# Optimization experiments

Hardware: AMD Instinct MI355X
Metric: run time of the kernel (lower is better)

Reference implementation:

```python
import jax, jax.numpy as jnp
import numpy as np

B = 4096   # batch_size from init_kwargs
D = 128    # embedding dim
TEMP = 0.25


def _l2_normalize(x, eps=1e-12):
    # matches F.normalize(dim=1): x / max(||x||, eps)
    n = jnp.linalg.norm(x, axis=1, keepdims=True)
    return x / jnp.maximum(n, eps)


def setup_inputs() -> dict:
    key = jax.random.key(0)
    k1, k2 = jax.random.split(key)
    return {
        "emb_i": jax.random.normal(k1, (B, D), dtype=jnp.float32),
        "emb_j": jax.random.normal(k2, (B, D), dtype=jnp.float32),
    }


def reference(emb_i, emb_j):
    b = emb_i.shape[0]
    z_i = _l2_normalize(emb_i)
    z_j = _l2_normalize(emb_j)
    reps = jnp.concatenate([z_i, z_j], axis=0)            # [2B, D]
    # cosine similarity of normalized vectors == dot product
    sim = reps @ reps.T                                    # [2B, 2B]
    sim_ij = jnp.diagonal(sim, offset=b)                   # [B]
    sim_ji = jnp.diagonal(sim, offset=-b)                  # [B]
    positives = jnp.concatenate([sim_ij, sim_ji], axis=0)  # [2B]
    # negatives_mask as overwritten in __init__: ones only on the two
    # off-diagonal cross-view blocks.
    mask = (
        jnp.zeros((2 * b, 2 * b), dtype=sim.dtype)
        .at[:b, b:].set(1.0)
        .at[b:, :b].set(1.0)
    )
    exp_sim = jnp.exp(sim / TEMP)                          # [2B, 2B]
    denom = jnp.sum(mask * exp_sim, axis=1)                # [2B]
    loss_partial = -jnp.log(jnp.exp(positives / TEMP) / denom)
    loss = jnp.sum(loss_partial) / (2 * b)
    return loss
```

## Files before the change

### kernel.cpp

```cpp
#include <hip/hip_runtime.h>

#define BATCH 4096
#define DIM   128
#define NT    32
#define EXP_SCALE 5.770780163555854f

typedef __bf16 bf16_t;
typedef __bf16 bf16x8 __attribute__((ext_vector_type(8)));
typedef float  f32x4  __attribute__((ext_vector_type(4)));

__global__ __launch_bounds__(256) void normalize_kernel(
    const float* __restrict__ emb_i, const float* __restrict__ emb_j,
    bf16_t* __restrict__ zi, bf16_t* __restrict__ zj, float* __restrict__ pos,
    float* __restrict__ denoms )
{
    if (blockIdx.x < 8) {
        int idx = (blockIdx.x * 256 + threadIdx.x) * 4;
        *(float4*)&denoms[idx] = make_float4(0.f, 0.f, 0.f, 0.f);
    }

    int wave = threadIdx.x >> 6;
    int lane = threadIdx.x & 63;
    int k = blockIdx.x * 4 + wave;

    const float2* ei = (const float2*)(emb_i + (size_t)k * DIM);
    const float2* ej = (const float2*)(emb_j + (size_t)k * DIM);
    float2 a = ei[lane];
    float2 b = ej[lane];

    float sii = a.x * a.x + a.y * a.y;
    float sjj = b.x * b.x + b.y * b.y;
    float sij = a.x * b.x + a.y * b.y;
#pragma unroll
    for (int m = 1; m < 64; m <<= 1) {
        sii += __shfl_xor(sii, m);
        sjj += __shfl_xor(sjj, m);
        sij += __shfl_xor(sij, m);
    }
    float inv_i = 1.0f / fmaxf(sqrtf(sii), 1e-12f);
    float inv_j = 1.0f / fmaxf(sqrtf(sjj), 1e-12f);

    struct bf16_2 { bf16_t x, y; };
    bf16_2 pi, pj;
    pi.x = (bf16_t)(a.x * inv_i);  pi.y = (bf16_t)(a.y * inv_i);
    pj.x = (bf16_t)(b.x * inv_j);  pj.y = (bf16_t)(b.y * inv_j);
    ((bf16_2*)(zi + (size_t)k * DIM))[lane] = pi;
    ((bf16_2*)(zj + (size_t)k * DIM))[lane] = pj;

    if (lane == 0) pos[k] = sij * inv_i * inv_j;
}

__global__ __launch_bounds__(256) void gemm_exp_kernel(
    const bf16_t* __restrict__ zi, const bf16_t* __restrict__ zj,
    float* __restrict__ rowDenom, float* __restrict__ colDenom)
{
    __shared__ __align__(16) bf16_t zi_s[128][136];
    __shared__ __align__(16) bf16_t zj_s[128][136];
    __shared__ float colRed[4][128];

    const int tid = threadIdx.x;
    const int ti = blockIdx.x, tj = blockIdx.y;

#pragma unroll
    for (int it = 0; it < 8; ++it) {
        int c = it * 256 + tid;
        int row = c >> 4;
        int col = (c & 15) << 3;
        *(uint4*)&zi_s[row][col] =
            *(const uint4*)(zi + ((size_t)(ti * 128 + row)) * DIM + col);
        *(uint4*)&zj_s[row][col] =
            *(const uint4*)(zj + ((size_t)(tj * 128 + row)) * DIM + col);
    }
    __syncthreads();

    const int wave = tid >> 6;
    const int lane = tid & 63;
    const int l15  = lane & 15;
    const int quad = lane >> 4;

    const f32x4 vzero = {0.f, 0.f, 0.f, 0.f};
    f32x4 acc[2][8];
#pragma unroll
    for (int rt = 0; rt < 2; ++rt)
#pragma unroll
        for (int ct = 0; ct < 8; ++ct) acc[rt][ct] = vzero;

#pragma unroll
    for (int ks = 0; ks < 4; ++ks) {
        int k0 = ks * 32 + quad * 8;
        bf16x8 afrag[2], bfrag[8];
#pragma unroll
        for (int rt = 0; rt < 2; ++rt)
            afrag[rt] = *(const bf16x8*)&zi_s[(wave * 2 + rt) * 16 + l15][k0];
#pragma unroll
        for (int ct = 0; ct < 8; ++ct)
            bfrag[ct] = *(const bf16x8*)&zj_s[ct * 16 + l15][k0];
#pragma unroll
        for (int rt = 0; rt < 2; ++rt)
#pragma unroll
            for (int ct = 0; ct < 8; ++ct)
                acc[rt][ct] = __builtin_amdgcn_mfma_f32_16x16x32_bf16(
                    afrag[rt], bfrag[ct], acc[rt][ct], 0, 0, 0);
    }

    float rowPart[2][4] = {{0.f, 0.f, 0.f, 0.f}, {0.f, 0.f, 0.f, 0.f}};
    float colPart[8]    = {0.f, 0.f, 0.f, 0.f, 0.f, 0.f, 0.f, 0.f};
#pragma unroll
    for (int rt = 0; rt < 2; ++rt)
#pragma unroll
        for (int ct = 0; ct < 8; ++ct)
#pragma unroll
            for (int r = 0; r < 4; ++r) {
                float e = exp2f(acc[rt][ct][r] * EXP_SCALE);
                rowPart[rt][r] += e;
                colPart[ct]    += e;
            }

#pragma unroll
    for (int rt = 0; rt < 2; ++rt)
#pragma unroll
        for (int r = 0; r < 4; ++r) {
            float v = rowPart[rt][r];
            v += __shfl_xor(v, 1);
            v += __shfl_xor(v, 2);
            v += __shfl_xor(v, 4);
            v += __shfl_xor(v, 8);
            if (l15 == 0) {
                int grow = ti * 128 + (wave * 2 + rt) * 16 + quad * 4 + r;
                atomicAdd(&rowDenom[grow], v);
            }
        }

#pragma unroll
    for (int ct = 0; ct < 8; ++ct) {
        float v = colPart[ct];
        v += __shfl_xor(v, 16);
        v += __shfl_xor(v, 32);
        if (quad == 0) colRed[wave][ct * 16 + l15] = v;
    }
    __syncthreads();
    if (tid < 128) {
        float s = colRed[0][tid] + colRed[1][tid] + colRed[2][tid] + colRed[3][tid];
        atomicAdd(&colDenom[tj * 128 + tid], s);
    }
}

__global__ __launch_bounds__(1024) void finalize_kernel(
    const float* __restrict__ denoms, const float* __restrict__ pos,
    float* __restrict__ out)
{
    const float4* rowD4 = (const float4*)denoms;
    const float4* colD4 = (const float4*)(denoms + BATCH);
    const float4* pos4  = (const float4*)pos;

    const int tid  = threadIdx.x;
    const int lane = tid & 63;
    const int wv   = tid >> 6;

    float4 rd = rowD4[tid];
    float4 cd = colD4[tid];
    float4 p  = pos4[tid];

    float acc = logf(rd.x) + logf(rd.y) + logf(rd.z) + logf(rd.w)
              + logf(cd.x) + logf(cd.y) + logf(cd.z) + logf(cd.w)
              - 8.0f * (p.x + p.y + p.z + p.w);

#pragma unroll
    for (int m = 1; m < 64; m <<= 1) acc += __shfl_xor(acc, m);

    __shared__ float red[16];
    if (lane == 0) red[wv] = acc;
    __syncthreads();
    if (wv == 0) {
        float v = (lane < 16) ? red[lane] : 0.0f;
#pragma unroll
        for (int m = 1; m < 64; m <<= 1) v += __shfl_xor(v, m);
        if (lane == 0) out[0] = v * (1.0f / (2.0f * BATCH));
    }
}

extern "C" void kernel_launch(void* const* d_in, const int* in_sizes, int n_in,
                              void* d_out, int out_size, void* d_ws, size_t ws_size,
                              hipStream_t stream) {
    const float* emb_i = (const float*)d_in[0];
    const float* emb_j = (const float*)d_in[1];
    float* out = (float*)d_out;

    char* ws = (char*)d_ws;
    bf16_t* zi     = (bf16_t*)(ws);
    bf16_t* zj     = (bf16_t*)(ws + (1u << 20));
    float*  denoms = (float*)(ws + (2u << 20));
    float*  pos    = denoms + 2 * BATCH;

    normalize_kernel<<<BATCH / 4, 256, 0, stream>>>(emb_i, emb_j, zi, zj, pos, denoms);
    gemm_exp_kernel<<<dim3(NT, NT), 256, 0, stream>>>(zi, zj, denoms, denoms + BATCH);
    finalize_kernel<<<1, 1024, 0, stream>>>(denoms, pos, out);
}
```

Before: 74.38 us.

## Enlarge GEMM-exp tiles to 256x256 with 512 threads and block-level row reduction

The fused similarity/exp kernel moves from 128x128 tiles with 256 threads to 256x256 tiles with 512 threads (8 waves in a 2x4 grid), so the grid shrinks from 1024 to 256 blocks. Row partial sums now go through shared memory before one atomic per row per block, which cuts global atomics and the number of times each operand is reloaded. In exchange, each block uses about 140KB of LDS plus larger accumulator and fragment register sets. That lowers occupancy and leaves only 256 blocks, roughly one per CU, which risks less latency hiding and load imbalance. The __launch_bounds__ annotation is also dropped.

```diff
diff --git a/kernel.cpp b/kernel.cpp
--- a/kernel.cpp
+++ b/kernel.cpp
@@ -2,7 +2,8 @@
 
 #define BATCH 4096
 #define DIM   128
-#define NT    32
+#define TILE  256
+#define NT    16
 #define EXP_SCALE 5.770780163555854f
 
 typedef __bf16 bf16_t;
@@ -50,26 +51,27 @@
     if (lane == 0) pos[k] = sij * inv_i * inv_j;
 }
 
-__global__ __launch_bounds__(256) void gemm_exp_kernel(
+__global__ void gemm_exp_kernel(
     const bf16_t* __restrict__ zi, const bf16_t* __restrict__ zj,
     float* __restrict__ rowDenom, float* __restrict__ colDenom)
 {
-    __shared__ __align__(16) bf16_t zi_s[128][136];
-    __shared__ __align__(16) bf16_t zj_s[128][136];
-    __shared__ float colRed[4][128];
+    __shared__ __align__(16) bf16_t zi_s[TILE][136];
+    __shared__ __align__(16) bf16_t zj_s[TILE][136];
+    __shared__ float rowRed[4][TILE];
+    __shared__ float colRed[2][TILE];
 
     const int tid = threadIdx.x;
     const int ti = blockIdx.x, tj = blockIdx.y;
 
 #pragma unroll
     for (int it = 0; it < 8; ++it) {
-        int c = it * 256 + tid;
+        int c = it * 512 + tid;
         int row = c >> 4;
         int col = (c & 15) << 3;
         *(uint4*)&zi_s[row][col] =
-            *(const uint4*)(zi + ((size_t)(ti * 128 + row)) * DIM + col);
+            *(const uint4*)(zi + ((size_t)(ti * TILE + row)) * DIM + col);
         *(uint4*)&zj_s[row][col] =
-            *(const uint4*)(zj + ((size_t)(tj * 128 + row)) * DIM + col);
+            *(const uint4*)(zj + ((size_t)(tj * TILE + row)) * DIM + col);
     }
     __syncthreads();
 
@@ -77,71 +79,79 @@
     const int lane = tid & 63;
     const int l15  = lane & 15;
     const int quad = lane >> 4;
+    const int wr   = wave >> 2;
+    const int wc   = wave & 3;
 
     const f32x4 vzero = {0.f, 0.f, 0.f, 0.f};
-    f32x4 acc[2][8];
-#pragma unroll
-    for (int rt = 0; rt < 2; ++rt)
-#pragma unroll
-        for (int ct = 0; ct < 8; ++ct) acc[rt][ct] = vzero;
+    f32x4 acc[8][4];
+#pragma unroll
+    for (int mr = 0; mr < 8; ++mr)
+#pragma unroll
+        for (int nc = 0; nc < 4; ++nc) acc[mr][nc] = vzero;
 
 #pragma unroll
     for (int ks = 0; ks < 4; ++ks) {
         int k0 = ks * 32 + quad * 8;
-        bf16x8 afrag[2], bfrag[8];
-#pragma unroll
-        for (int rt = 0; rt < 2; ++rt)
-            afrag[rt] = *(const bf16x8*)&zi_s[(wave * 2 + rt) * 16 + l15][k0];
-#pragma unroll
-        for (int ct = 0; ct < 8; ++ct)
-            bfrag[ct] = *(const bf16x8*)&zj_s[ct * 16 + l15][k0];
-#pragma unroll
-        for (int rt = 0; rt < 2; ++rt)
-#pragma unroll
-            for (int ct = 0; ct < 8; ++ct)
-                acc[rt][ct] = __builtin_amdgcn_mfma_f32_16x16x32_bf16(
-                    afrag[rt], bfrag[ct], acc[rt][ct], 0, 0, 0);
-    }
-
-    float rowPart[2][4] = {{0.f, 0.f, 0.f, 0.f}, {0.f, 0.f, 0.f, 0.f}};
-    float colPart[8]    = {0.f, 0.f, 0.f, 0.f, 0.f, 0.f, 0.f, 0.f};
-#pragma unroll
-    for (int rt = 0; rt < 2; ++rt)
-#pragma unroll
-        for (int ct = 0; ct < 8; ++ct)
+        bf16x8 afrag[8], bfrag[4];
+#pragma unroll
+        for (int mr = 0; mr < 8; ++mr)
+            afrag[mr] = *(const bf16x8*)&zi_s[wr * 128 + mr * 16 + l15][k0];
+#pragma unroll
+        for (int nc = 0; nc < 4; ++nc)
+            bfrag[nc] = *(const bf16x8*)&zj_s[wc * 64 + nc * 16 + l15][k0];
+#pragma unroll
+        for (int mr = 0; mr < 8; ++mr)
+#pragma unroll
+            for (int nc = 0; nc < 4; ++nc)
+                acc[mr][nc] = __builtin_amdgcn_mfma_f32_16x16x32_bf16(
+                    afrag[mr], bfrag[nc], acc[mr][nc], 0, 0, 0);
+    }
+
+    float rowPart[8][4];
+    float colPart[4] = {0.f, 0.f, 0.f, 0.f};
+#pragma unroll
+    for (int mr = 0; mr < 8; ++mr)
+#pragma unroll
+        for (int r = 0; r < 4; ++r) rowPart[mr][r] = 0.f;
+
+#pragma unroll
+    for (int mr = 0; mr < 8; ++mr)
+#pragma unroll
+        for (int nc = 0; nc < 4; ++nc)
 #pragma unroll
             for (int r = 0; r < 4; ++r) {
-                float e = exp2f(acc[rt][ct][r] * EXP_SCALE);
-                rowPart[rt][r] += e;
-                colPart[ct]    += e;
+                float e = exp2f(acc[mr][nc][r] * EXP_SCALE);
+                rowPart[mr][r] += e;
+                colPart[nc]    += e;
             }
 
 #pragma unroll
-    for (int rt = 0; rt < 2; ++rt)
+    for (int mr = 0; mr < 8; ++mr)
 #pragma unroll
         for (int r = 0; r < 4; ++r) {
-            float v = rowPart[rt][r];
+            float v = rowPart[mr][r];
             v += __shfl_xor(v, 1);
             v += __shfl_xor(v, 2);
             v += __shfl_xor(v, 4);
             v += __shfl_xor(v, 8);
-            if (l15 == 0) {
-                int grow = ti * 128 + (wave * 2 + rt) * 16 + quad * 4 + r;
-                atomicAdd(&rowDenom[grow], v);
-            }
+            if (l15 == 0)
+                rowRed[wc][wr * 128 + mr * 16 + quad * 4 + r] = v;
         }
 
 #pragma unroll
-    for (int ct = 0; ct < 8; ++ct) {
-        float v = colPart[ct];
+    for (int nc = 0; nc < 4; ++nc) {
+        float v = colPart[nc];
         v += __shfl_xor(v, 16);
         v += __shfl_xor(v, 32);
-        if (quad == 0) colRed[wave][ct * 16 + l15] = v;
+        if (quad == 0) colRed[wr][wc * 64 + nc * 16 + l15] = v;
     }
     __syncthreads();
-    if (tid < 128) {
-        float s = colRed[0][tid] + colRed[1][tid] + colRed[2][tid] + colRed[3][tid];
-        atomicAdd(&colDenom[tj * 128 + tid], s);
+
+    if (tid < TILE) {
+        float rs = rowRed[0][tid] + rowRed[1][tid] + rowRed[2][tid] + rowRed[3][tid];
+        atomicAdd(&rowDenom[ti * TILE + tid], rs);
+        float cs = colRed[0][tid] + colRed[1][tid];
+        atomicAdd(&colDenom[tj * TILE + tid], cs);
     }
 }
 
@@ -193,6 +203,6 @@
     float*  pos    = denoms + 2 * BATCH;
 
     normalize_kernel<<<BATCH / 4, 256, 0, stream>>>(emb_i, emb_j, zi, zj, pos, denoms);
-    gemm_exp_kernel<<<dim3(NT, NT), 256, 0, stream>>>(zi, zj, denoms, denoms + BATCH);
+    gemm_exp_kernel<<<dim3(NT, NT), 512, 0, stream>>>(zi, zj, denoms, denoms + BATCH);
     finalize_kernel<<<1, 1024, 0, stream>>>(denoms, pos, out);
 }
```

Measured after the change: 118.9 us. +59.8%, slower.
